# Optimization experiments

Hardware: AMD Instinct MI355X
Metric: run time of the kernel (lower is better)

The kernel has to match this reference:

```python
import jax, jax.numpy as jnp
import numpy as np

N_NODES = 20000
N_EDGES = 640000

def _graph_conv(x, edge_index, w_rel, b_rel, w_root):
    # PyG GraphConv (aggr='add'): out = lin_rel(sum_{j in N(i)} x_j) + lin_root(x_i)
    src, dst = edge_index[0], edge_index[1]
    agg = jax.ops.segment_sum(x[src], dst, num_segments=x.shape[0])  # [N, d_in]
    return agg @ w_rel + b_rel + x @ w_root


def setup_inputs() -> dict:
    key = jax.random.key(0)
    ks = jax.random.split(key, 12)
    def glorot(k, shape):
        lim = float(np.sqrt(6.0 / (shape[0] + shape[1])))
        return jax.random.uniform(k, shape, jnp.float32, -lim, lim)
    x = jax.random.normal(ks[0], (N_NODES, 128), dtype=jnp.float32)
    edge_index = jax.random.randint(ks[1], (2, N_EDGES), 0, N_NODES, dtype=jnp.int64)
    return {
        "x": x,
        "edge_index": edge_index,
        "w_rel1": glorot(ks[2], (128, 64)),
        "b_rel1": jnp.zeros((64,), jnp.float32),
        "w_root1": glorot(ks[3], (128, 64)),
        "w_l1": glorot(ks[4], (64, 32)),
        "b_l1": jnp.zeros((32,), jnp.float32),
        "w_rel2": glorot(ks[5], (32, 16)),
        "b_rel2": jnp.zeros((16,), jnp.float32),
        "w_root2": glorot(ks[6], (32, 16)),
        "w_l2": glorot(ks[7], (16, 10)),
        "b_l2": jnp.zeros((10,), jnp.float32),
    }


def reference(x, edge_index, w_rel1, b_rel1, w_root1, w_l1, b_l1,
              w_rel2, b_rel2, w_root2, w_l2, b_l2):
    h = _graph_conv(x, edge_index, w_rel1, b_rel1, w_root1)   # [N, 64]
    h = jax.nn.relu(h @ w_l1 + b_l1)                          # [N, 32]
    h = _graph_conv(h, edge_index, w_rel2, b_rel2, w_root2)   # [N, 16]
    h = h @ w_l2 + b_l2                                       # [N, 10]
    return jax.nn.log_softmax(h, axis=1)
```

## Files before the change

### kernel.cpp

```cpp
#include <hip/hip_runtime.h>
#include <math.h>

#define N_NODES 20000
#define N_EDGES 640000
#define CAP 96

__global__ __launch_bounds__(256) void compose_zero(
    const float* __restrict__ w_rel1, const float* __restrict__ b_rel1,
    const float* __restrict__ w_root1,
    const float* __restrict__ w_l1, const float* __restrict__ b_l1,
    const float* __restrict__ w_rel2, const float* __restrict__ b_rel2,
    const float* __restrict__ w_root2,
    const float* __restrict__ w_l2, const float* __restrict__ b_l2,
    float* __restrict__ P1, float* __restrict__ Q1, float* __restrict__ c1,
    float* __restrict__ W2r, float* __restrict__ W2o, float* __restrict__ c2,
    int* __restrict__ cnt)
{
    const int b = blockIdx.x, t = threadIdx.x;
    if (b < 32) {
        const bool isP = (b < 16);
        const int idx = (isP ? b : b - 16) * 256 + t;
        const int k = idx >> 5, j = idx & 31;
        const float* wsrc = isP ? w_rel1 : w_root1;
        float s = 0.f;
        #pragma unroll 8
        for (int m = 0; m < 64; ++m) s += wsrc[k * 64 + m] * w_l1[m * 32 + j];
        (isP ? P1 : Q1)[idx] = s;
    } else if (b == 32) {
        for (int i = t; i < 512; i += 256) {
            const int k = i >> 4, j = i & 15;
            float sr = 0.f, so = 0.f;
            if (j < 10) {
                #pragma unroll
                for (int m = 0; m < 16; ++m) {
                    sr += w_rel2[k * 16 + m] * w_l2[m * 10 + j];
                    so += w_root2[k * 16 + m] * w_l2[m * 10 + j];
                }
            }
            W2r[i] = sr;
            W2o[i] = so;
        }
        if (t < 32) {
            float s = b_l1[t];
            #pragma unroll 8
            for (int m = 0; m < 64; ++m) s += b_rel1[m] * w_l1[m * 32 + t];
            c1[t] = s;
        }
        if (t < 16) {
            float s = 0.f;
            if (t < 10) {
                s = b_l2[t];
                #pragma unroll
                for (int m = 0; m < 16; ++m) s += b_rel2[m] * w_l2[m * 10 + t];
            }
            c2[t] = s;
        }
    } else {
        const int i = (b - 33) * 256 + t;
        if (i < N_NODES) cnt[i] = 0;
    }
}

__global__ __launch_bounds__(256) void fill_bucket(
    const int* __restrict__ ei, int* __restrict__ cnt,
    int* __restrict__ esrc)
{
    const int t = blockIdx.x * 256 + threadIdx.x;
    const int2* sp = (const int2*)ei;
    const int2* dp = (const int2*)(ei + N_EDGES);
    const int2 sa = sp[t * 2];
    const int2 sb = sp[t * 2 + 1];
    const int2 da = dp[t * 2];
    const int2 db = dp[t * 2 + 1];
    const int p0 = atomicAdd(&cnt[da.x], 1);
    const int p1 = atomicAdd(&cnt[da.y], 1);
    const int p2 = atomicAdd(&cnt[db.x], 1);
    const int p3 = atomicAdd(&cnt[db.y], 1);
    if (p0 < CAP) esrc[da.x * CAP + p0] = sa.x;
    if (p1 < CAP) esrc[da.y * CAP + p1] = sa.y;
    if (p2 < CAP) esrc[db.x * CAP + p2] = sb.x;
    if (p3 < CAP) esrc[db.y * CAP + p3] = sb.y;
}

__global__ __launch_bounds__(256) void proj1(
    const float* __restrict__ x, const float* __restrict__ P1,
    const float* __restrict__ Q1, const float* __restrict__ c1,
    float* __restrict__ a, float* __restrict__ r)
{
    __shared__ float s_W[128 * 64];
    for (int i = threadIdx.x; i < 128 * 64; i += 256) {
        const int k = i >> 6, j = i & 63;
        s_W[i] = (j < 32) ? P1[k * 32 + j] : Q1[k * 32 + (j - 32)];
    }
    __syncthreads();

    const int wave = threadIdx.x >> 6;
    const int lane = threadIdx.x & 63;
    const int f = lane & 31;
    const float cadd = (lane >= 32) ? c1[f] : 0.f;

    const int n0 = blockIdx.x * 16 + wave * 4;
    const float4* xp0 = (const float4*)(x + (n0 + 0) * 128);
    const float4* xp1 = (const float4*)(x + (n0 + 1) * 128);
    const float4* xp2 = (const float4*)(x + (n0 + 2) * 128);
    const float4* xp3 = (const float4*)(x + (n0 + 3) * 128);
    float a0 = 0.f, a1 = 0.f, a2 = 0.f, a3 = 0.f;
    #pragma unroll 8
    for (int k4 = 0; k4 < 32; ++k4) {
        const float4 va = xp0[k4], vb = xp1[k4], vc = xp2[k4], vd = xp3[k4];
        const int kb = k4 * 4;
        {
            const float w = s_W[(kb + 0) * 64 + lane];
            a0 += va.x * w; a1 += vb.x * w; a2 += vc.x * w; a3 += vd.x * w;
        }
        {
            const float w = s_W[(kb + 1) * 64 + lane];
            a0 += va.y * w; a1 += vb.y * w; a2 += vc.y * w; a3 += vd.y * w;
        }
        {
            const float w = s_W[(kb + 2) * 64 + lane];
            a0 += va.z * w; a1 += vb.z * w; a2 += vc.z * w; a3 += vd.z * w;
        }
        {
            const float w = s_W[(kb + 3) * 64 + lane];
            a0 += va.w * w; a1 += vb.w * w; a2 += vc.w * w; a3 += vd.w * w;
        }
    }
    if (lane < 32) {
        a[(n0 + 0) * 32 + f] = a0;
        a[(n0 + 1) * 32 + f] = a1;
        a[(n0 + 2) * 32 + f] = a2;
        a[(n0 + 3) * 32 + f] = a3;
    } else {
        r[(n0 + 0) * 32 + f] = a0 + cadd;
        r[(n0 + 1) * 32 + f] = a1 + cadd;
        r[(n0 + 2) * 32 + f] = a2 + cadd;
        r[(n0 + 3) * 32 + f] = a3 + cadd;
    }
}

__global__ __launch_bounds__(256) void agg1_mlp(
    const int* __restrict__ cnt, const int* __restrict__ esrc,
    const float* __restrict__ a, const float* __restrict__ r,
    const float* __restrict__ W2r, const float* __restrict__ W2o,
    const float* __restrict__ c2,
    float* __restrict__ hw, float* __restrict__ g2l)
{
    __shared__ float s_W2[1024];
    for (int i = threadIdx.x; i < 1024; i += 256)
        s_W2[i] = (i < 512) ? W2r[i] : W2o[i - 512];
    __syncthreads();

    const int wave = threadIdx.x >> 6;
    const int lane = threadIdx.x & 63;
    const int epar = lane >> 5;
    const int f = lane & 31;
    const int d = blockIdx.x * 4 + wave;

    const int beg = d * CAP;
    const int deg = min(cnt[d], CAP);
    float acc = (epar == 0) ? r[d * 32 + f] : 0.f;
    int done = 0;
    while (done < deg) {
        const int m = min(64, deg - done);
        int eid = 0;
        if (lane < m) eid = esrc[beg + done + lane];
        #pragma unroll 4
        for (int t = 0; t < m; t += 2) {
            const int k = t + epar;
            const int s = __shfl(eid, k);
            if (k < m) acc += a[s * 32 + f];
        }
        done += m;
    }
    acc += __shfl_xor(acc, 32);
    const float h2 = fmaxf(acc, 0.f);

    float o = (epar == 1 && f < 16) ? c2[f] : 0.f;
    #pragma unroll 8
    for (int k = 0; k < 32; ++k) {
        const float hk = __shfl(h2, k, 32);
        if (f < 16) o += hk * s_W2[epar * 512 + k * 16 + f];
    }
    if (f < 16) {
        if (epar == 0) hw[d * 16 + f] = o;
        else           g2l[d * 16 + f] = o;
    }
}

__global__ __launch_bounds__(256) void agg2_head(
    const int* __restrict__ cnt, const int* __restrict__ esrc,
    const float* __restrict__ hw, const float* __restrict__ g2l,
    float* __restrict__ out)
{
    const int g = threadIdx.x >> 4;
    const int f = threadIdx.x & 15;
    const int d = blockIdx.x * 16 + g;

    const int beg = d * CAP;
    const int deg = min(cnt[d], CAP);
    float acc = g2l[d * 16 + f];
    int done = 0;
    while (done < deg) {
        const int m = min(16, deg - done);
        int eid = 0;
        if (f < m) eid = esrc[beg + done + f];
        #pragma unroll 4
        for (int k = 0; k < m; ++k) {
            const int s = __shfl(eid, k, 16);
            acc += hw[s * 16 + f];
        }
        done += m;
    }
    float mv = (f < 10) ? acc : -INFINITY;
    #pragma unroll
    for (int off = 8; off > 0; off >>= 1) mv = fmaxf(mv, __shfl_xor(mv, off, 16));
    float ev = (f < 10) ? expf(acc - mv) : 0.f;
    #pragma unroll
    for (int off = 8; off > 0; off >>= 1) ev += __shfl_xor(ev, off, 16);
    const float lse = mv + logf(ev);
    if (f < 10) out[d * 10 + f] = acc - lse;
}

extern "C" void kernel_launch(void* const* d_in, const int* in_sizes, int n_in,
                              void* d_out, int out_size, void* d_ws, size_t ws_size,
                              hipStream_t stream) {
    const float* x       = (const float*)d_in[0];
    const int*   ei      = (const int*)d_in[1];
    const float* w_rel1  = (const float*)d_in[2];
    const float* b_rel1  = (const float*)d_in[3];
    const float* w_root1 = (const float*)d_in[4];
    const float* w_l1    = (const float*)d_in[5];
    const float* b_l1    = (const float*)d_in[6];
    const float* w_rel2  = (const float*)d_in[7];
    const float* b_rel2  = (const float*)d_in[8];
    const float* w_root2 = (const float*)d_in[9];
    const float* w_l2    = (const float*)d_in[10];
    const float* b_l2    = (const float*)d_in[11];
    float* out = (float*)d_out;

    float* ws   = (float*)d_ws;
    float* a    = ws;
    float* r    = ws + 640000;
    float* hw   = ws + 1280000;
    float* g2l  = ws + 1600000;
    float* P1   = ws + 1920000;
    float* Q1   = ws + 1924096;
    float* c1   = ws + 1928192;
    float* W2r  = ws + 1928224;
    float* W2o  = ws + 1928736;
    float* c2   = ws + 1929248;
    int* ibase  = (int*)(ws + 1929264);
    int* cnt    = ibase;
    int* esrc   = ibase + 20000;

    compose_zero<<<112, 256, 0, stream>>>(w_rel1, b_rel1, w_root1, w_l1, b_l1,
                                          w_rel2, b_rel2, w_root2, w_l2, b_l2,
                                          P1, Q1, c1, W2r, W2o, c2, cnt);

    fill_bucket<<<625, 256, 0, stream>>>(ei, cnt, esrc);

    proj1<<<1250, 256, 0, stream>>>(x, P1, Q1, c1, a, r);

    agg1_mlp<<<5000, 256, 0, stream>>>(cnt, esrc, a, r, W2r, W2o, c2, hw, g2l);

    agg2_head<<<1250, 256, 0, stream>>>(cnt, esrc, hw, g2l, out);
}
```

Measured before the change: 189.0 us.

## Merge bucket fill with projection and restructure edge gathers with scalar indices

Merges the independent bucket-fill and layer-1 projection kernels into one launch, so the atomic fill and the GEMV-like projection can overlap on the device and one launch is saved. Both aggregation kernels now read edge indices through wave-uniform scalar loads (readfirstlane) instead of cooperative loads plus shuffles. agg2_head is rebuilt to give each node a full wave, with four edge-parity groups per wave and a cross-group reduction. The trade is a larger grid and partly idle lanes in agg2_head in exchange for more memory-level parallelism and fewer shuffles.

```diff
diff --git a/kernel.cpp b/kernel.cpp
--- a/kernel.cpp
+++ b/kernel.cpp
@@ -61,81 +61,79 @@
     }
 }
 
-__global__ __launch_bounds__(256) void fill_bucket(
-    const int* __restrict__ ei, int* __restrict__ cnt,
-    int* __restrict__ esrc)
-{
-    const int t = blockIdx.x * 256 + threadIdx.x;
-    const int2* sp = (const int2*)ei;
-    const int2* dp = (const int2*)(ei + N_EDGES);
-    const int2 sa = sp[t * 2];
-    const int2 sb = sp[t * 2 + 1];
-    const int2 da = dp[t * 2];
-    const int2 db = dp[t * 2 + 1];
-    const int p0 = atomicAdd(&cnt[da.x], 1);
-    const int p1 = atomicAdd(&cnt[da.y], 1);
-    const int p2 = atomicAdd(&cnt[db.x], 1);
-    const int p3 = atomicAdd(&cnt[db.y], 1);
-    if (p0 < CAP) esrc[da.x * CAP + p0] = sa.x;
-    if (p1 < CAP) esrc[da.y * CAP + p1] = sa.y;
-    if (p2 < CAP) esrc[db.x * CAP + p2] = sb.x;
-    if (p3 < CAP) esrc[db.y * CAP + p3] = sb.y;
-}
-
-__global__ __launch_bounds__(256) void proj1(
+__global__ __launch_bounds__(256) void fill_proj(
+    const int* __restrict__ ei, int* __restrict__ cnt, int* __restrict__ esrc,
     const float* __restrict__ x, const float* __restrict__ P1,
     const float* __restrict__ Q1, const float* __restrict__ c1,
     float* __restrict__ a, float* __restrict__ r)
 {
     __shared__ float s_W[128 * 64];
-    for (int i = threadIdx.x; i < 128 * 64; i += 256) {
-        const int k = i >> 6, j = i & 63;
-        s_W[i] = (j < 32) ? P1[k * 32 + j] : Q1[k * 32 + (j - 32)];
-    }
-    __syncthreads();
-
-    const int wave = threadIdx.x >> 6;
-    const int lane = threadIdx.x & 63;
-    const int f = lane & 31;
-    const float cadd = (lane >= 32) ? c1[f] : 0.f;
-
-    const int n0 = blockIdx.x * 16 + wave * 4;
-    const float4* xp0 = (const float4*)(x + (n0 + 0) * 128);
-    const float4* xp1 = (const float4*)(x + (n0 + 1) * 128);
-    const float4* xp2 = (const float4*)(x + (n0 + 2) * 128);
-    const float4* xp3 = (const float4*)(x + (n0 + 3) * 128);
-    float a0 = 0.f, a1 = 0.f, a2 = 0.f, a3 = 0.f;
-    #pragma unroll 8
-    for (int k4 = 0; k4 < 32; ++k4) {
-        const float4 va = xp0[k4], vb = xp1[k4], vc = xp2[k4], vd = xp3[k4];
-        const int kb = k4 * 4;
-        {
-            const float w = s_W[(kb + 0) * 64 + lane];
-            a0 += va.x * w; a1 += vb.x * w; a2 += vc.x * w; a3 += vd.x * w;
-        }
-        {
-            const float w = s_W[(kb + 1) * 64 + lane];
-            a0 += va.y * w; a1 += vb.y * w; a2 += vc.y * w; a3 += vd.y * w;
-        }
-        {
-            const float w = s_W[(kb + 2) * 64 + lane];
-            a0 += va.z * w; a1 += vb.z * w; a2 += vc.z * w; a3 += vd.z * w;
-        }
-        {
-            const float w = s_W[(kb + 3) * 64 + lane];
-            a0 += va.w * w; a1 += vb.w * w; a2 += vc.w * w; a3 += vd.w * w;
-        }
-    }
-    if (lane < 32) {
-        a[(n0 + 0) * 32 + f] = a0;
-        a[(n0 + 1) * 32 + f] = a1;
-        a[(n0 + 2) * 32 + f] = a2;
-        a[(n0 + 3) * 32 + f] = a3;
+    if (blockIdx.x < 625) {
+        const int t = blockIdx.x * 256 + threadIdx.x;
+        const int2* sp = (const int2*)ei;
+        const int2* dp = (const int2*)(ei + N_EDGES);
+        const int2 sa = sp[t * 2];
+        const int2 sb = sp[t * 2 + 1];
+        const int2 da = dp[t * 2];
+        const int2 db = dp[t * 2 + 1];
+        const int p0 = atomicAdd(&cnt[da.x], 1);
+        const int p1 = atomicAdd(&cnt[da.y], 1);
+        const int p2 = atomicAdd(&cnt[db.x], 1);
+        const int p3 = atomicAdd(&cnt[db.y], 1);
+        if (p0 < CAP) esrc[da.x * CAP + p0] = sa.x;
+        if (p1 < CAP) esrc[da.y * CAP + p1] = sa.y;
+        if (p2 < CAP) esrc[db.x * CAP + p2] = sb.x;
+        if (p3 < CAP) esrc[db.y * CAP + p3] = sb.y;
     } else {
-        r[(n0 + 0) * 32 + f] = a0 + cadd;
-        r[(n0 + 1) * 32 + f] = a1 + cadd;
-        r[(n0 + 2) * 32 + f] = a2 + cadd;
-        r[(n0 + 3) * 32 + f] = a3 + cadd;
+        for (int i = threadIdx.x; i < 128 * 64; i += 256) {
+            const int k = i >> 6, j = i & 63;
+            s_W[i] = (j < 32) ? P1[k * 32 + j] : Q1[k * 32 + (j - 32)];
+        }
+        __syncthreads();
+
+        const int wave = threadIdx.x >> 6;
+        const int lane = threadIdx.x & 63;
+        const int f = lane & 31;
+        const float cadd = (lane >= 32) ? c1[f] : 0.f;
+
+        const int n0 = (blockIdx.x - 625) * 16 + wave * 4;
+        const float4* xp0 = (const float4*)(x + (n0 + 0) * 128);
+        const float4* xp1 = (const float4*)(x + (n0 + 1) * 128);
+        const float4* xp2 = (const float4*)(x + (n0 + 2) * 128);
+        const float4* xp3 = (const float4*)(x + (n0 + 3) * 128);
+        float a0 = 0.f, a1 = 0.f, a2 = 0.f, a3 = 0.f;
+        #pragma unroll 8
+        for (int k4 = 0; k4 < 32; ++k4) {
+            const float4 va = xp0[k4], vb = xp1[k4], vc = xp2[k4], vd = xp3[k4];
+            const int kb = k4 * 4;
+            {
+                const float w = s_W[(kb + 0) * 64 + lane];
+                a0 += va.x * w; a1 += vb.x * w; a2 += vc.x * w; a3 += vd.x * w;
+            }
+            {
+                const float w = s_W[(kb + 1) * 64 + lane];
+                a0 += va.y * w; a1 += vb.y * w; a2 += vc.y * w; a3 += vd.y * w;
+            }
+            {
+                const float w = s_W[(kb + 2) * 64 + lane];
+                a0 += va.z * w; a1 += vb.z * w; a2 += vc.z * w; a3 += vd.z * w;
+            }
+            {
+                const float w = s_W[(kb + 3) * 64 + lane];
+                a0 += va.w * w; a1 += vb.w * w; a2 += vc.w * w; a3 += vd.w * w;
+            }
+        }
+        if (lane < 32) {
+            a[(n0 + 0) * 32 + f] = a0;
+            a[(n0 + 1) * 32 + f] = a1;
+            a[(n0 + 2) * 32 + f] = a2;
+            a[(n0 + 3) * 32 + f] = a3;
+        } else {
+            r[(n0 + 0) * 32 + f] = a0 + cadd;
+            r[(n0 + 1) * 32 + f] = a1 + cadd;
+            r[(n0 + 2) * 32 + f] = a2 + cadd;
+            r[(n0 + 3) * 32 + f] = a3 + cadd;
+        }
     }
 }
 
@@ -157,30 +155,30 @@
     const int f = lane & 31;
     const int d = blockIdx.x * 4 + wave;
 
-    const int beg = d * CAP;
-    const int deg = min(cnt[d], CAP);
+    const int beg = __builtin_amdgcn_readfirstlane(d * CAP);
+    const int deg = __builtin_amdgcn_readfirstlane(min(cnt[d], CAP));
+
     float acc = (epar == 0) ? r[d * 32 + f] : 0.f;
-    int done = 0;
-    while (done < deg) {
-        const int m = min(64, deg - done);
-        int eid = 0;
-        if (lane < m) eid = esrc[beg + done + lane];
-        #pragma unroll 4
-        for (int t = 0; t < m; t += 2) {
-            const int k = t + epar;
-            const int s = __shfl(eid, k);
-            if (k < m) acc += a[s * 32 + f];
-        }
-        done += m;
+    int k = 0;
+    #pragma unroll 4
+    for (; k + 1 < deg; k += 2) {
+        const int s0 = esrc[beg + k];
+        const int s1 = esrc[beg + k + 1];
+        const int ss = (epar == 0) ? s0 : s1;
+        acc += a[ss * 32 + f];
+    }
+    if (k < deg) {
+        const int sl = esrc[beg + k];
+        if (epar == 0) acc += a[sl * 32 + f];
     }
     acc += __shfl_xor(acc, 32);
     const float h2 = fmaxf(acc, 0.f);
 
     float o = (epar == 1 && f < 16) ? c2[f] : 0.f;
     #pragma unroll 8
-    for (int k = 0; k < 32; ++k) {
-        const float hk = __shfl(h2, k, 32);
-        if (f < 16) o += hk * s_W2[epar * 512 + k * 16 + f];
+    for (int k2 = 0; k2 < 32; ++k2) {
+        const float hk = __shfl(h2, k2, 32);
+        if (f < 16) o += hk * s_W2[epar * 512 + k2 * 16 + f];
     }
     if (f < 16) {
         if (epar == 0) hw[d * 16 + f] = o;
@@ -193,25 +191,39 @@
     const float* __restrict__ hw, const float* __restrict__ g2l,
     float* __restrict__ out)
 {
-    const int g = threadIdx.x >> 4;
-    const int f = threadIdx.x & 15;
-    const int d = blockIdx.x * 16 + g;
-
-    const int beg = d * CAP;
-    const int deg = min(cnt[d], CAP);
-    float acc = g2l[d * 16 + f];
-    int done = 0;
-    while (done < deg) {
-        const int m = min(16, deg - done);
-        int eid = 0;
-        if (f < m) eid = esrc[beg + done + f];
-        #pragma unroll 4
-        for (int k = 0; k < m; ++k) {
-            const int s = __shfl(eid, k, 16);
-            acc += hw[s * 16 + f];
-        }
-        done += m;
-    }
+    const int wave = threadIdx.x >> 6;
+    const int lane = threadIdx.x & 63;
+    const int epar = lane >> 4;
+    const int f = lane & 15;
+    const int d = blockIdx.x * 4 + wave;
+
+    const int beg = __builtin_amdgcn_readfirstlane(d * CAP);
+    const int deg = __builtin_amdgcn_readfirstlane(min(cnt[d], CAP));
+
+    float acc = (epar == 0) ? g2l[d * 16 + f] : 0.f;
+    int k = 0;
+    #pragma unroll 2
+    for (; k + 3 < deg; k += 4) {
+        const int s0 = esrc[beg + k];
+        const int s1 = esrc[beg + k + 1];
+        const int s2 = esrc[beg + k + 2];
+        const int s3 = esrc[beg + k + 3];
+        const int ssA = (epar & 1) ? s1 : s0;
+        const int ssB = (epar & 1) ? s3 : s2;
+        const int ss = (epar & 2) ? ssB : ssA;
+        acc += hw[ss * 16 + f];
+    }
+    const int rem = deg - k;
+    if (rem > 0) { const int s0 = esrc[beg + k];
+                   if (epar == 0) acc += hw[s0 * 16 + f]; }
+    if (rem > 1) { const int s1 = esrc[beg + k + 1];
+                   if (epar == 1) acc += hw[s1 * 16 + f]; }
+    if (rem > 2) { const int s2 = esrc[beg + k + 2];
+                   if (epar == 2) acc += hw[s2 * 16 + f]; }
+
+    acc += __shfl_xor(acc, 16);
+    acc += __shfl_xor(acc, 32);
+
     float mv = (f < 10) ? acc : -INFINITY;
     #pragma unroll
     for (int off = 8; off > 0; off >>= 1) mv = fmaxf(mv, __shfl_xor(mv, off, 16));
@@ -219,7 +231,7 @@
     #pragma unroll
     for (int off = 8; off > 0; off >>= 1) ev += __shfl_xor(ev, off, 16);
     const float lse = mv + logf(ev);
-    if (f < 10) out[d * 10 + f] = acc - lse;
+    if (epar == 0 && f < 10) out[d * 10 + f] = acc - lse;
 }
 
 extern "C" void kernel_launch(void* const* d_in, const int* in_sizes, int n_in,
@@ -258,11 +270,9 @@
                                           w_rel2, b_rel2, w_root2, w_l2, b_l2,
                                           P1, Q1, c1, W2r, W2o, c2, cnt);
 
-    fill_bucket<<<625, 256, 0, stream>>>(ei, cnt, esrc);
-
-    proj1<<<1250, 256, 0, stream>>>(x, P1, Q1, c1, a, r);
+    fill_proj<<<1875, 256, 0, stream>>>(ei, cnt, esrc, x, P1, Q1, c1, a, r);
 
     agg1_mlp<<<5000, 256, 0, stream>>>(cnt, esrc, a, r, W2r, W2o, c2, hw, g2l);
 
-    agg2_head<<<1250, 256, 0, stream>>>(cnt, esrc, hw, g2l, out);
-}
+    agg2_head<<<5000, 256, 0, stream>>>(cnt, esrc, hw, g2l, out);
+}
```

Measured after the change: 174.3 us. 1.08x faster.
